# Performance work log

Hardware: AMD Instinct MI355X
Metric: run time of the kernel (lower is better)

Reference implementation:

```python
import jax, jax.numpy as jnp
import numpy as np

N_NODES = 100000
N_EDGES = 1600000
F_IN = 128
DIM = 64
N_CLASSES = 40


def setup_inputs() -> dict:
    key = jax.random.key(0)
    ks = jax.random.split(key, 12)
    x = jax.random.normal(ks[0], (N_NODES, F_IN), dtype=jnp.float32)
    edge_index = jax.random.randint(ks[1], (2, N_EDGES), 0, N_NODES, dtype=jnp.int64)
    s = lambda fan_in: 1.0 / np.sqrt(fan_in)
    W1 = jax.random.uniform(ks[2], (F_IN, DIM), jnp.float32, -s(F_IN), s(F_IN))
    b1 = jax.random.uniform(ks[3], (DIM,), jnp.float32, -s(F_IN), s(F_IN))
    W2 = jax.random.uniform(ks[4], (DIM, DIM), jnp.float32, -s(DIM), s(DIM))
    b2 = jax.random.uniform(ks[5], (DIM,), jnp.float32, -s(DIM), s(DIM))
    Wf1 = jax.random.uniform(ks[6], (DIM, DIM), jnp.float32, -s(DIM), s(DIM))
    bf1 = jax.random.uniform(ks[7], (DIM,), jnp.float32, -s(DIM), s(DIM))
    Wf2 = jax.random.uniform(ks[8], (DIM, N_CLASSES), jnp.float32, -s(DIM), s(DIM))
    bf2 = jax.random.uniform(ks[9], (N_CLASSES,), jnp.float32, -s(DIM), s(DIM))
    return {"x": x, "edge_index": edge_index, "W1": W1, "b1": b1,
            "W2": W2, "b2": b2, "Wf1": Wf1, "bf1": bf1, "Wf2": Wf2, "bf2": bf2}


def _gin_agg(h, src, dst, n_nodes):
    # sum_{j in N(i)} h_j : gather along src, scatter-add to dst
    return jax.ops.segment_sum(h[src], dst, num_segments=n_nodes)


def reference(x, edge_index, W1, b1, W2, b2, Wf1, bf1, Wf2, bf2):
    src, dst = edge_index[0], edge_index[1]
    n = x.shape[0]
    # GINConv(Linear), eps=0: Linear(x + sum_neighbors)
    h = jax.nn.relu((x + _gin_agg(x, src, dst, n)) @ W1 + b1)
    h = jax.nn.relu((h + _gin_agg(h, src, dst, n)) @ W2 + b2)
    h = jax.nn.relu(h @ Wf1 + bf1)  # dropout p=0.5 is identity at inference
    logits = h @ Wf2 + bf2
    return jax.nn.log_softmax(logits, axis=1)
```

## Files before the change

kernel.cpp:

```cpp
#include <hip/hip_runtime.h>

#define NN 100000
#define NE 1600000
#define F_IN 128
#define DIM 64
#define NC 40
#define NB 196
#define MAXBE 10240

typedef unsigned short ushort_t;
typedef __attribute__((ext_vector_type(8))) short bf16x8;
typedef __attribute__((ext_vector_type(4))) float f32x4;

static __device__ __forceinline__ float b2f(ushort_t u) {
  return __uint_as_float(((unsigned)u) << 16);
}
static __device__ __forceinline__ ushort_t f2b(float f) {
  unsigned x = __float_as_uint(f);
  return (ushort_t)((x + 0x7fffu + ((x >> 16) & 1u)) >> 16);
}
static __device__ __forceinline__ unsigned pack2(float a, float b) {
  return (unsigned)f2b(a) | ((unsigned)f2b(b) << 16);
}

__global__ __launch_bounds__(256) void k_prep(const float* __restrict__ W1,
                                              const float* __restrict__ W2,
                                              const float* __restrict__ Wf1,
                                              const float* __restrict__ Wf2,
                                              ushort_t* __restrict__ W1T,
                                              ushort_t* __restrict__ W2T,
                                              ushort_t* __restrict__ Wf1T,
                                              ushort_t* __restrict__ Wf2T,
                                              int* __restrict__ bcur) {
  int t = threadIdx.x;
  if (t < NB) bcur[t] = 0;
  for (int i = t; i < 64 * 128; i += 256) { int c = i >> 7, k = i & 127; W1T[i] = f2b(W1[k * 64 + c]); }
  for (int i = t; i < 64 * 64; i += 256)  { int c = i >> 6, k = i & 63;  W2T[i] = f2b(W2[k * 64 + c]); }
  for (int i = t; i < 64 * 64; i += 256)  { int c = i >> 6, k = i & 63;  Wf1T[i] = f2b(Wf1[k * 64 + c]); }
  for (int i = t; i < 48 * 64; i += 256)  { int c = i >> 6, k = i & 63;  Wf2T[i] = (c < NC) ? f2b(Wf2[k * NC + c]) : (ushort_t)0; }
}

__global__ __launch_bounds__(512) void k_part(const int* __restrict__ src,
                                              const int* __restrict__ dst,
                                              int* __restrict__ bcur,
                                              unsigned* __restrict__ part) {
  __shared__ int hist[NB];
  __shared__ int gbase[NB];
  int t = threadIdx.x;
  for (int i = t; i < NB; i += 512) hist[i] = 0;
  __syncthreads();
  int e0 = blockIdx.x * 4096;
  int s[8], dd[8], r[8];
#pragma unroll
  for (int i = 0; i < 8; ++i) {
    int e = e0 + i * 512 + t;
    if (e < NE) {
      dd[i] = dst[e];
      s[i] = src[e];
      r[i] = atomicAdd(&hist[dd[i] >> 9], 1);
    }
  }
  __syncthreads();
  for (int i = t; i < NB; i += 512)
    gbase[i] = hist[i] ? atomicAdd(&bcur[i], hist[i]) : 0;
  __syncthreads();
#pragma unroll
  for (int i = 0; i < 8; ++i) {
    int e = e0 + i * 512 + t;
    if (e < NE) {
      int b = dd[i] >> 9;
      part[(size_t)b * MAXBE + gbase[b] + r[i]] = ((unsigned)(dd[i] & 511) << 17) | (unsigned)s[i];
    }
  }
}

__global__ __launch_bounds__(512) void k_csr(const int* __restrict__ bcur,
                                             const unsigned* __restrict__ part,
                                             int* __restrict__ cnt,
                                             int* __restrict__ offs,
                                             int* __restrict__ slots) {
  __shared__ unsigned pb[MAXBE];
  __shared__ ushort_t rk[MAXBE];
  __shared__ int lcnt[512];
  __shared__ int loff[512];
  int b = blockIdx.x, t = threadIdx.x;
  int start = b * MAXBE;
  int m = bcur[b];
  if (m > MAXBE) m = MAXBE;
  lcnt[t] = 0;
  __syncthreads();
  for (int i = t; i < m; i += 512) {
    unsigned v = part[start + i];
    pb[i] = v;
    rk[i] = (ushort_t)atomicAdd(&lcnt[v >> 17], 1);
  }
  __syncthreads();
  int o0 = lcnt[t];
  __syncthreads();
  for (int off = 1; off < 512; off <<= 1) {
    int u = (t >= off) ? lcnt[t - off] : 0;
    __syncthreads();
    lcnt[t] += u;
    __syncthreads();
  }
  int excl = lcnt[t] - o0;
  loff[t] = excl;
  int gn = (b << 9) + t;
  if (gn < NN) { cnt[gn] = o0; offs[gn] = start + excl; }
  __syncthreads();
  for (int i = t; i < m; i += 512) {
    unsigned v = pb[i];
    slots[start + loff[v >> 17] + rk[i]] = (int)(v & 0x1FFFFu);
  }
}

__global__ __launch_bounds__(256) void k_agg(const ushort_t* __restrict__ yb,
                                             const int* __restrict__ cnt,
                                             const int* __restrict__ offs,
                                             const int* __restrict__ slots,
                                             const float* __restrict__ bias,
                                             ushort_t* __restrict__ hb) {
  int wv = threadIdx.x >> 6, l = threadIdx.x & 63;
  int h = l >> 5;
  int n = blockIdx.x * 8 + wv * 2 + h;
  int li = l & 31;
  int g = (l >> 3) & 3;
  int q = l & 7;
  unsigned cb = (unsigned)q * 16u;
  int deg = cnt[n], start = offs[n];
  deg = deg > 64 ? 64 : deg;
  int sv0 = (li < deg) ? slots[start + li] : 0;
  int sv1 = (32 + li < deg) ? slots[start + 32 + li] : 0;
  int dego = __shfl_xor(deg, 32);
  int degmax = deg > dego ? deg : dego;
  float acc[8];
#pragma unroll
  for (int i = 0; i < 8; ++i) acc[i] = 0.f;
  const char* ybp = (const char*)yb;
  int hbase = h << 5;
  for (int j = 0; j < degmax; j += 16) {
    int i0 = j + g, i1 = j + 4 + g, i2 = j + 8 + g, i3 = j + 12 + g;
    int sa, sb, sc, sd;
    if (j < 32) {
      sa = __shfl(sv0, hbase + i0); sb = __shfl(sv0, hbase + i1);
      sc = __shfl(sv0, hbase + i2); sd = __shfl(sv0, hbase + i3);
    } else {
      sa = __shfl(sv1, hbase + (i0 & 31)); sb = __shfl(sv1, hbase + (i1 & 31));
      sc = __shfl(sv1, hbase + (i2 & 31)); sd = __shfl(sv1, hbase + (i3 & 31));
    }
    uint4 u0 = {0,0,0,0}, u1 = {0,0,0,0}, u2 = {0,0,0,0}, u3 = {0,0,0,0};
    if (i0 < deg) u0 = *(const uint4*)(ybp + ((unsigned)sa * 128u + cb));
    if (i1 < deg) u1 = *(const uint4*)(ybp + ((unsigned)sb * 128u + cb));
    if (i2 < deg) u2 = *(const uint4*)(ybp + ((unsigned)sc * 128u + cb));
    if (i3 < deg) u3 = *(const uint4*)(ybp + ((unsigned)sd * 128u + cb));
    acc[0] += __uint_as_float(u0.x << 16);  acc[1] += __uint_as_float(u0.x);
    acc[2] += __uint_as_float(u0.y << 16);  acc[3] += __uint_as_float(u0.y);
    acc[4] += __uint_as_float(u0.z << 16);  acc[5] += __uint_as_float(u0.z);
    acc[6] += __uint_as_float(u0.w << 16);  acc[7] += __uint_as_float(u0.w);
    acc[0] += __uint_as_float(u1.x << 16);  acc[1] += __uint_as_float(u1.x);
    acc[2] += __uint_as_float(u1.y << 16);  acc[3] += __uint_as_float(u1.y);
    acc[4] += __uint_as_float(u1.z << 16);  acc[5] += __uint_as_float(u1.z);
    acc[6] += __uint_as_float(u1.w << 16);  acc[7] += __uint_as_float(u1.w);
    acc[0] += __uint_as_float(u2.x << 16);  acc[1] += __uint_as_float(u2.x);
    acc[2] += __uint_as_float(u2.y << 16);  acc[3] += __uint_as_float(u2.y);
    acc[4] += __uint_as_float(u2.z << 16);  acc[5] += __uint_as_float(u2.z);
    acc[6] += __uint_as_float(u2.w << 16);  acc[7] += __uint_as_float(u2.w);
    acc[0] += __uint_as_float(u3.x << 16);  acc[1] += __uint_as_float(u3.x);
    acc[2] += __uint_as_float(u3.y << 16);  acc[3] += __uint_as_float(u3.y);
    acc[4] += __uint_as_float(u3.z << 16);  acc[5] += __uint_as_float(u3.z);
    acc[6] += __uint_as_float(u3.w << 16);  acc[7] += __uint_as_float(u3.w);
  }
#pragma unroll
  for (int i = 0; i < 8; ++i) {
    acc[i] += __shfl_xor(acc[i], 8);
    acc[i] += __shfl_xor(acc[i], 16);
  }
  if (li < 8) {
    uint4 yr = *(const uint4*)(ybp + ((unsigned)n * 128u + (unsigned)q * 16u));
    float4 ba = *(const float4*)&bias[q * 8];
    float4 bb = *(const float4*)&bias[q * 8 + 4];
    float v0 = fmaxf(__uint_as_float(yr.x << 16)         + acc[0] + ba.x, 0.f);
    float v1 = fmaxf(__uint_as_float(yr.x & 0xffff0000u) + acc[1] + ba.y, 0.f);
    float v2 = fmaxf(__uint_as_float(yr.y << 16)         + acc[2] + ba.z, 0.f);
    float v3 = fmaxf(__uint_as_float(yr.y & 0xffff0000u) + acc[3] + ba.w, 0.f);
    float v4 = fmaxf(__uint_as_float(yr.z << 16)         + acc[4] + bb.x, 0.f);
    float v5 = fmaxf(__uint_as_float(yr.z & 0xffff0000u) + acc[5] + bb.y, 0.f);
    float v6 = fmaxf(__uint_as_float(yr.w << 16)         + acc[6] + bb.z, 0.f);
    float v7 = fmaxf(__uint_as_float(yr.w & 0xffff0000u) + acc[7] + bb.w, 0.f);
    uint4 st;
    st.x = pack2(v0, v1);
    st.y = pack2(v2, v3);
    st.z = pack2(v4, v5);
    st.w = pack2(v6, v7);
    *(uint4*)&hb[(size_t)n * 64 + q * 8] = st;
  }
}

__global__ __launch_bounds__(256) void k_gemm1(const float* __restrict__ x,
                                               const ushort_t* __restrict__ W1T,
                                               ushort_t* __restrict__ yb) {
  __shared__ ushort_t H[64 * 136];
  int t = threadIdx.x, w = t >> 6, l = t & 63;
  int g = l >> 4, r16 = l & 15;
  int node0 = blockIdx.x * 64;
  bf16x8 B[4][4];
#pragma unroll
  for (int nt = 0; nt < 4; ++nt)
#pragma unroll
    for (int kt = 0; kt < 4; ++kt)
      B[nt][kt] = *(const bf16x8*)&W1T[(16 * nt + r16) * 128 + 32 * kt + 8 * g];
#pragma unroll
  for (int j = 0; j < 8; ++j) {
    int f = t + 256 * j;
    int e = f * 4;
    int n = e >> 7, c = e & 127;
    int gn = node0 + n; if (gn >= NN) gn = NN - 1;
    float4 v = *(const float4*)&x[(size_t)gn * 128 + c];
    ushort4 pv;
    pv.x = f2b(v.x); pv.y = f2b(v.y); pv.z = f2b(v.z); pv.w = f2b(v.w);
    *(ushort4*)&H[n * 136 + c] = pv;
  }
  __syncthreads();
  f32x4 acc[4] = {{0.f,0.f,0.f,0.f},{0.f,0.f,0.f,0.f},{0.f,0.f,0.f,0.f},{0.f,0.f,0.f,0.f}};
#pragma unroll
  for (int kt = 0; kt < 4; ++kt) {
    bf16x8 A = *(const bf16x8*)&H[(16 * w + r16) * 136 + 32 * kt + 8 * g];
#pragma unroll
    for (int nt = 0; nt < 4; ++nt)
      acc[nt] = __builtin_amdgcn_mfma_f32_16x16x32_bf16(A, B[nt][kt], acc[nt], 0, 0, 0);
  }
#pragma unroll
  for (int nt = 0; nt < 4; ++nt)
#pragma unroll
    for (int i = 0; i < 4; ++i) {
      int node = node0 + 16 * w + 4 * g + i;
      if (node < NN)
        yb[(size_t)node * 64 + 16 * nt + r16] = f2b(acc[nt][i]);
    }
}

__global__ __launch_bounds__(256) void k_mid(const ushort_t* __restrict__ hb,
                                             const ushort_t* __restrict__ W2T,
                                             ushort_t* __restrict__ yb) {
  __shared__ ushort_t H[64 * 72];
  int t = threadIdx.x, w = t >> 6, l = t & 63;
  int g = l >> 4, r16 = l & 15;
  int node0 = blockIdx.x * 64;
  bf16x8 B[4][2];
#pragma unroll
  for (int nt = 0; nt < 4; ++nt)
#pragma unroll
    for (int kt = 0; kt < 2; ++kt)
      B[nt][kt] = *(const bf16x8*)&W2T[(16 * nt + r16) * 64 + 32 * kt + 8 * g];
#pragma unroll
  for (int j = 0; j < 2; ++j) {
    int i = t + 256 * j;
    int n = i >> 3, c8 = (i & 7) * 8;
    int gn = node0 + n; if (gn >= NN) gn = NN - 1;
    uint4 u = *(const uint4*)&hb[(size_t)gn * 64 + c8];
    *(uint4*)&H[n * 72 + c8] = u;
  }
  __syncthreads();
  f32x4 acc[4] = {{0.f,0.f,0.f,0.f},{0.f,0.f,0.f,0.f},{0.f,0.f,0.f,0.f},{0.f,0.f,0.f,0.f}};
#pragma unroll
  for (int kt = 0; kt < 2; ++kt) {
    bf16x8 A = *(const bf16x8*)&H[(16 * w + r16) * 72 + 32 * kt + 8 * g];
#pragma unroll
    for (int nt = 0; nt < 4; ++nt)
      acc[nt] = __builtin_amdgcn_mfma_f32_16x16x32_bf16(A, B[nt][kt], acc[nt], 0, 0, 0);
  }
#pragma unroll
  for (int nt = 0; nt < 4; ++nt)
#pragma unroll
    for (int i = 0; i < 4; ++i) {
      int node = node0 + 16 * w + 4 * g + i;
      if (node < NN)
        yb[(size_t)node * 64 + 16 * nt + r16] = f2b(acc[nt][i]);
    }
}

__global__ __launch_bounds__(256) void k_final(const ushort_t* __restrict__ hb,
                                               const ushort_t* __restrict__ Wf1T,
                                               const float* __restrict__ bf1,
                                               const ushort_t* __restrict__ Wf2T,
                                               const float* __restrict__ bf2,
                                               float* __restrict__ out) {
  __shared__ ushort_t H[64 * 72];
  __shared__ ushort_t H2[64 * 72];
  int t = threadIdx.x, w = t >> 6, l = t & 63;
  int g = l >> 4, r16 = l & 15;
  int node0 = blockIdx.x * 64;
  bf16x8 B1[4][2], B2[3][2];
#pragma unroll
  for (int nt = 0; nt < 4; ++nt)
#pragma unroll
    for (int kt = 0; kt < 2; ++kt)
      B1[nt][kt] = *(const bf16x8*)&Wf1T[(16 * nt + r16) * 64 + 32 * kt + 8 * g];
#pragma unroll
  for (int nt = 0; nt < 3; ++nt)
#pragma unroll
    for (int kt = 0; kt < 2; ++kt)
      B2[nt][kt] = *(const bf16x8*)&Wf2T[(16 * nt + r16) * 64 + 32 * kt + 8 * g];
#pragma unroll
  for (int j = 0; j < 2; ++j) {
    int i = t + 256 * j;
    int n = i >> 3, c8 = (i & 7) * 8;
    int gn = node0 + n; if (gn >= NN) gn = NN - 1;
    uint4 u = *(const uint4*)&hb[(size_t)gn * 64 + c8];
    *(uint4*)&H[n * 72 + c8] = u;
  }
  __syncthreads();
  f32x4 acc[4] = {{0.f,0.f,0.f,0.f},{0.f,0.f,0.f,0.f},{0.f,0.f,0.f,0.f},{0.f,0.f,0.f,0.f}};
#pragma unroll
  for (int kt = 0; kt < 2; ++kt) {
    bf16x8 A = *(const bf16x8*)&H[(16 * w + r16) * 72 + 32 * kt + 8 * g];
#pragma unroll
    for (int nt = 0; nt < 4; ++nt)
      acc[nt] = __builtin_amdgcn_mfma_f32_16x16x32_bf16(A, B1[nt][kt], acc[nt], 0, 0, 0);
  }
#pragma unroll
  for (int nt = 0; nt < 4; ++nt) {
    float bias = bf1[16 * nt + r16];
#pragma unroll
    for (int i = 0; i < 4; ++i) {
      float v = fmaxf(acc[nt][i] + bias, 0.f);
      H2[(16 * w + 4 * g + i) * 72 + 16 * nt + r16] = f2b(v);
    }
  }
  __syncthreads();
  f32x4 acc2[3] = {{0.f,0.f,0.f,0.f},{0.f,0.f,0.f,0.f},{0.f,0.f,0.f,0.f}};
#pragma unroll
  for (int kt = 0; kt < 2; ++kt) {
    bf16x8 A2 = *(const bf16x8*)&H2[(16 * w + r16) * 72 + 32 * kt + 8 * g];
#pragma unroll
    for (int nt = 0; nt < 3; ++nt)
      acc2[nt] = __builtin_amdgcn_mfma_f32_16x16x32_bf16(A2, B2[nt][kt], acc2[nt], 0, 0, 0);
  }
  float lg[3][4];
#pragma unroll
  for (int nt = 0; nt < 3; ++nt) {
    int col = 16 * nt + r16;
    float bias = (col < NC) ? bf2[col] : 0.f;
#pragma unroll
    for (int i = 0; i < 4; ++i)
      lg[nt][i] = (col < NC) ? acc2[nt][i] + bias : -1e30f;
  }
#pragma unroll
  for (int i = 0; i < 4; ++i) {
    float m = fmaxf(fmaxf(lg[0][i], lg[1][i]), lg[2][i]);
#pragma unroll
    for (int off = 1; off < 16; off <<= 1) m = fmaxf(m, __shfl_xor(m, off));
    float s = 0.f;
#pragma unroll
    for (int nt = 0; nt < 3; ++nt)
      s += (lg[nt][i] > -1e29f) ? __expf(lg[nt][i] - m) : 0.f;
#pragma unroll
    for (int off = 1; off < 16; off <<= 1) s += __shfl_xor(s, off);
    float ls = __logf(s);
    int node = node0 + 16 * w + 4 * g + i;
#pragma unroll
    for (int nt = 0; nt < 3; ++nt) {
      int col = 16 * nt + r16;
      if (col < NC && node < NN)
        out[(size_t)node * NC + col] = lg[nt][i] - m - ls;
    }
  }
}

extern "C" void kernel_launch(void* const* d_in, const int* in_sizes, int n_in,
                              void* d_out, int out_size, void* d_ws, size_t ws_size,
                              hipStream_t stream) {
  const float* x   = (const float*)d_in[0];
  const int*   ei  = (const int*)d_in[1];
  const float* W1  = (const float*)d_in[2];
  const float* b1  = (const float*)d_in[3];
  const float* W2  = (const float*)d_in[4];
  const float* b2  = (const float*)d_in[5];
  const float* Wf1 = (const float*)d_in[6];
  const float* bf1 = (const float*)d_in[7];
  const float* Wf2 = (const float*)d_in[8];
  const float* bf2 = (const float*)d_in[9];
  float* out = (float*)d_out;

  char* ws = (char*)d_ws;
  size_t o = 0;
  int* bcur  = (int*)(ws + o); o += 4096;
  int* cnt   = (int*)(ws + o); o += 400000;
  int* offs  = (int*)(ws + o); o += 400000;
  o = (o + 255) & ~(size_t)255;
  ushort_t* W1T  = (ushort_t*)(ws + o); o += 64 * 128 * 2;
  ushort_t* W2T  = (ushort_t*)(ws + o); o += 64 * 64 * 2;
  ushort_t* Wf1T = (ushort_t*)(ws + o); o += 64 * 64 * 2;
  ushort_t* Wf2T = (ushort_t*)(ws + o); o += 48 * 64 * 2;
  o = (o + 255) & ~(size_t)255;
  unsigned* part = (unsigned*)(ws + o); o += (size_t)NB * MAXBE * 4;
  int* slots = (int*)(ws + o); o += (size_t)NB * MAXBE * 4;
  ushort_t* yb = (ushort_t*)(ws + o); o += (size_t)NN * DIM * 2;
  ushort_t* hb = (ushort_t*)(ws + o); o += (size_t)NN * DIM * 2;

  const int* srcp = ei;
  const int* dstp = ei + NE;

  k_prep<<<1, 256, 0, stream>>>(W1, W2, Wf1, Wf2, W1T, W2T, Wf1T, Wf2T, bcur);
  k_part<<<(NE + 4095) / 4096, 512, 0, stream>>>(srcp, dstp, bcur, part);
  k_csr<<<NB, 512, 0, stream>>>(bcur, part, cnt, offs, slots);
  k_gemm1<<<(NN + 63) / 64, 256, 0, stream>>>(x, W1T, yb);
  k_agg<<<NN / 8, 256, 0, stream>>>(yb, cnt, offs, slots, b1, hb);
  k_mid<<<(NN + 63) / 64, 256, 0, stream>>>(hb, W2T, yb);
  k_agg<<<NN / 8, 256, 0, stream>>>(yb, cnt, offs, slots, b2, hb);
  k_final<<<(NN + 63) / 64, 256, 0, stream>>>(hb, Wf1T, bf1, Wf2T, bf2, out);
}
```

Baseline: 167.9 us.

## Merge edge partitioning and first GEMM into one launch, parallelize weight prep

The edge-bucketing kernel and the layer-1 projection GEMM, which are independent, now run in one launch: the first 391 blocks partition edges and the rest compute x@W1 into bf16. This removes a launch and lets the two memory-bound phases overlap on the GPU. The weight transpose/convert kernel is spread over 77 blocks instead of one, shortening that serial step. The partition blocks now use 256 threads with 16 edges each, which adds register pressure. That mix may affect occupancy for the GEMM path.

```diff
diff --git a/kernel.cpp b/kernel.cpp
--- a/kernel.cpp
+++ b/kernel.cpp
@@ -7,6 +7,7 @@
 #define NC 40
 #define NB 196
 #define MAXBE 10240
+#define NPB 391
 
 typedef unsigned short ushort_t;
 typedef __attribute__((ext_vector_type(8))) short bf16x8;
@@ -32,46 +33,102 @@
                                               ushort_t* __restrict__ Wf1T,
                                               ushort_t* __restrict__ Wf2T,
                                               int* __restrict__ bcur) {
+  int i = blockIdx.x * 256 + threadIdx.x;
+  if (i < 8192) {
+    int c = i >> 7, k = i & 127;
+    W1T[i] = f2b(W1[k * 64 + c]);
+  } else if (i < 12288) {
+    int j = i - 8192, c = j >> 6, k = j & 63;
+    W2T[j] = f2b(W2[k * 64 + c]);
+  } else if (i < 16384) {
+    int j = i - 12288, c = j >> 6, k = j & 63;
+    Wf1T[j] = f2b(Wf1[k * 64 + c]);
+  } else if (i < 19456) {
+    int j = i - 16384, c = j >> 6, k = j & 63;
+    Wf2T[j] = (c < NC) ? f2b(Wf2[k * NC + c]) : (ushort_t)0;
+  } else if (i < 19456 + NB) {
+    bcur[i - 19456] = 0;
+  }
+}
+
+__global__ __launch_bounds__(256) void k_pg(const int* __restrict__ src,
+                                            const int* __restrict__ dst,
+                                            int* __restrict__ bcur,
+                                            unsigned* __restrict__ part,
+                                            const float* __restrict__ x,
+                                            const ushort_t* __restrict__ W1T,
+                                            ushort_t* __restrict__ yb) {
+  __shared__ ushort_t H[64 * 136];
+  int bid = blockIdx.x;
   int t = threadIdx.x;
-  if (t < NB) bcur[t] = 0;
-  for (int i = t; i < 64 * 128; i += 256) { int c = i >> 7, k = i & 127; W1T[i] = f2b(W1[k * 64 + c]); }
-  for (int i = t; i < 64 * 64; i += 256)  { int c = i >> 6, k = i & 63;  W2T[i] = f2b(W2[k * 64 + c]); }
-  for (int i = t; i < 64 * 64; i += 256)  { int c = i >> 6, k = i & 63;  Wf1T[i] = f2b(Wf1[k * 64 + c]); }
-  for (int i = t; i < 48 * 64; i += 256)  { int c = i >> 6, k = i & 63;  Wf2T[i] = (c < NC) ? f2b(Wf2[k * NC + c]) : (ushort_t)0; }
-}
-
-__global__ __launch_bounds__(512) void k_part(const int* __restrict__ src,
-                                              const int* __restrict__ dst,
-                                              int* __restrict__ bcur,
-                                              unsigned* __restrict__ part) {
-  __shared__ int hist[NB];
-  __shared__ int gbase[NB];
-  int t = threadIdx.x;
-  for (int i = t; i < NB; i += 512) hist[i] = 0;
-  __syncthreads();
-  int e0 = blockIdx.x * 4096;
-  int s[8], dd[8], r[8];
-#pragma unroll
-  for (int i = 0; i < 8; ++i) {
-    int e = e0 + i * 512 + t;
-    if (e < NE) {
-      dd[i] = dst[e];
-      s[i] = src[e];
-      r[i] = atomicAdd(&hist[dd[i] >> 9], 1);
-    }
-  }
-  __syncthreads();
-  for (int i = t; i < NB; i += 512)
-    gbase[i] = hist[i] ? atomicAdd(&bcur[i], hist[i]) : 0;
-  __syncthreads();
-#pragma unroll
-  for (int i = 0; i < 8; ++i) {
-    int e = e0 + i * 512 + t;
-    if (e < NE) {
-      int b = dd[i] >> 9;
-      part[(size_t)b * MAXBE + gbase[b] + r[i]] = ((unsigned)(dd[i] & 511) << 17) | (unsigned)s[i];
-    }
-  }
+  if (bid < NPB) {
+    int* hist = (int*)H;
+    int* gbase = hist + NB;
+    for (int i = t; i < NB; i += 256) hist[i] = 0;
+    __syncthreads();
+    int e0 = bid * 4096;
+    int s[16], dd[16], r[16];
+#pragma unroll
+    for (int i = 0; i < 16; ++i) {
+      int e = e0 + i * 256 + t;
+      if (e < NE) {
+        dd[i] = dst[e];
+        s[i] = src[e];
+        r[i] = atomicAdd(&hist[dd[i] >> 9], 1);
+      }
+    }
+    __syncthreads();
+    for (int i = t; i < NB; i += 256)
+      gbase[i] = hist[i] ? atomicAdd(&bcur[i], hist[i]) : 0;
+    __syncthreads();
+#pragma unroll
+    for (int i = 0; i < 16; ++i) {
+      int e = e0 + i * 256 + t;
+      if (e < NE) {
+        int b = dd[i] >> 9;
+        part[(size_t)b * MAXBE + gbase[b] + r[i]] = ((unsigned)(dd[i] & 511) << 17) | (unsigned)s[i];
+      }
+    }
+    return;
+  }
+  int blk = bid - NPB;
+  int w = t >> 6, l = t & 63;
+  int g = l >> 4, r16 = l & 15;
+  int node0 = blk * 64;
+  bf16x8 B[4][4];
+#pragma unroll
+  for (int nt = 0; nt < 4; ++nt)
+#pragma unroll
+    for (int kt = 0; kt < 4; ++kt)
+      B[nt][kt] = *(const bf16x8*)&W1T[(16 * nt + r16) * 128 + 32 * kt + 8 * g];
+#pragma unroll
+  for (int j = 0; j < 8; ++j) {
+    int f = t + 256 * j;
+    int e = f * 4;
+    int n = e >> 7, c = e & 127;
+    int gn = node0 + n; if (gn >= NN) gn = NN - 1;
+    float4 v = *(const float4*)&x[(size_t)gn * 128 + c];
+    ushort4 pv;
+    pv.x = f2b(v.x); pv.y = f2b(v.y); pv.z = f2b(v.z); pv.w = f2b(v.w);
+    *(ushort4*)&H[n * 136 + c] = pv;
+  }
+  __syncthreads();
+  f32x4 acc[4] = {{0.f,0.f,0.f,0.f},{0.f,0.f,0.f,0.f},{0.f,0.f,0.f,0.f},{0.f,0.f,0.f,0.f}};
+#pragma unroll
+  for (int kt = 0; kt < 4; ++kt) {
+    bf16x8 A = *(const bf16x8*)&H[(16 * w + r16) * 136 + 32 * kt + 8 * g];
+#pragma unroll
+    for (int nt = 0; nt < 4; ++nt)
+      acc[nt] = __builtin_amdgcn_mfma_f32_16x16x32_bf16(A, B[nt][kt], acc[nt], 0, 0, 0);
+  }
+#pragma unroll
+  for (int nt = 0; nt < 4; ++nt)
+#pragma unroll
+    for (int i = 0; i < 4; ++i) {
+      int node = node0 + 16 * w + 4 * g + i;
+      if (node < NN)
+        yb[(size_t)node * 64 + 16 * nt + r16] = f2b(acc[nt][i]);
+    }
 }
 
 __global__ __launch_bounds__(512) void k_csr(const int* __restrict__ bcur,
@@ -196,49 +253,6 @@
   }
 }
 
-__global__ __launch_bounds__(256) void k_gemm1(const float* __restrict__ x,
-                                               const ushort_t* __restrict__ W1T,
-                                               ushort_t* __restrict__ yb) {
-  __shared__ ushort_t H[64 * 136];
-  int t = threadIdx.x, w = t >> 6, l = t & 63;
-  int g = l >> 4, r16 = l & 15;
-  int node0 = blockIdx.x * 64;
-  bf16x8 B[4][4];
-#pragma unroll
-  for (int nt = 0; nt < 4; ++nt)
-#pragma unroll
-    for (int kt = 0; kt < 4; ++kt)
-      B[nt][kt] = *(const bf16x8*)&W1T[(16 * nt + r16) * 128 + 32 * kt + 8 * g];
-#pragma unroll
-  for (int j = 0; j < 8; ++j) {
-    int f = t + 256 * j;
-    int e = f * 4;
-    int n = e >> 7, c = e & 127;
-    int gn = node0 + n; if (gn >= NN) gn = NN - 1;
-    float4 v = *(const float4*)&x[(size_t)gn * 128 + c];
-    ushort4 pv;
-    pv.x = f2b(v.x); pv.y = f2b(v.y); pv.z = f2b(v.z); pv.w = f2b(v.w);
-    *(ushort4*)&H[n * 136 + c] = pv;
-  }
-  __syncthreads();
-  f32x4 acc[4] = {{0.f,0.f,0.f,0.f},{0.f,0.f,0.f,0.f},{0.f,0.f,0.f,0.f},{0.f,0.f,0.f,0.f}};
-#pragma unroll
-  for (int kt = 0; kt < 4; ++kt) {
-    bf16x8 A = *(const bf16x8*)&H[(16 * w + r16) * 136 + 32 * kt + 8 * g];
-#pragma unroll
-    for (int nt = 0; nt < 4; ++nt)
-      acc[nt] = __builtin_amdgcn_mfma_f32_16x16x32_bf16(A, B[nt][kt], acc[nt], 0, 0, 0);
-  }
-#pragma unroll
-  for (int nt = 0; nt < 4; ++nt)
-#pragma unroll
-    for (int i = 0; i < 4; ++i) {
-      int node = node0 + 16 * w + 4 * g + i;
-      if (node < NN)
-        yb[(size_t)node * 64 + 16 * nt + r16] = f2b(acc[nt][i]);
-    }
-}
-
 __global__ __launch_bounds__(256) void k_mid(const ushort_t* __restrict__ hb,
                                              const ushort_t* __restrict__ W2T,
                                              ushort_t* __restrict__ yb) {
@@ -401,10 +415,9 @@
   const int* srcp = ei;
   const int* dstp = ei + NE;
 
-  k_prep<<<1, 256, 0, stream>>>(W1, W2, Wf1, Wf2, W1T, W2T, Wf1T, Wf2T, bcur);
-  k_part<<<(NE + 4095) / 4096, 512, 0, stream>>>(srcp, dstp, bcur, part);
+  k_prep<<<77, 256, 0, stream>>>(W1, W2, Wf1, Wf2, W1T, W2T, Wf1T, Wf2T, bcur);
+  k_pg<<<NPB + (NN + 63) / 64, 256, 0, stream>>>(srcp, dstp, bcur, part, x, W1T, yb);
   k_csr<<<NB, 512, 0, stream>>>(bcur, part, cnt, offs, slots);
-  k_gemm1<<<(NN + 63) / 64, 256, 0, stream>>>(x, W1T, yb);
   k_agg<<<NN / 8, 256, 0, stream>>>(yb, cnt, offs, slots, b1, hb);
   k_mid<<<(NN + 63) / 64, 256, 0, stream>>>(hb, W2T, yb);
   k_agg<<<NN / 8, 256, 0, stream>>>(yb, cnt, offs, slots, b2, hb);
```

Result: faster. 152.7 us (-9.0%).
